# Performance work log

Hardware: AMD Instinct MI355X
Metric: run time of the kernel (lower is better)

Reference implementation:

```python
import jax, jax.numpy as jnp
import numpy as np

NUM_EXPERTS = 7
TRUNK_DIM = 64
HIDDEN = 64   # max(48, trunk_dim)
NUM_DEPTH_CLASSES = 3
BATCH = 262144


def setup_inputs() -> dict:
    key = jax.random.key(0)
    ks = jax.random.split(key, 8)
    trunk_feat = jax.random.normal(ks[0], (BATCH, TRUNK_DIM), dtype=jnp.float32)
    size_idx = jax.random.randint(ks[1], (BATCH,), 0, NUM_EXPERTS, dtype=jnp.int64)
    # Stacked expert MLP params: Linear(64,64) -> ReLU -> Linear(64,64) -> ReLU -> Linear(64,3)
    s1 = 1.0 / np.sqrt(TRUNK_DIM)
    s2 = 1.0 / np.sqrt(HIDDEN)
    W1 = jax.random.uniform(ks[2], (NUM_EXPERTS, TRUNK_DIM, HIDDEN), jnp.float32, -s1, s1)
    b1 = jax.random.uniform(ks[3], (NUM_EXPERTS, HIDDEN), jnp.float32, -s1, s1)
    W2 = jax.random.uniform(ks[4], (NUM_EXPERTS, HIDDEN, HIDDEN), jnp.float32, -s2, s2)
    b2 = jax.random.uniform(ks[5], (NUM_EXPERTS, HIDDEN), jnp.float32, -s2, s2)
    W3 = jax.random.uniform(ks[6], (NUM_EXPERTS, HIDDEN, NUM_DEPTH_CLASSES), jnp.float32, -s2, s2)
    b3 = jax.random.uniform(ks[7], (NUM_EXPERTS, NUM_DEPTH_CLASSES), jnp.float32, -s2, s2)
    return {"trunk_feat": trunk_feat, "size_idx": size_idx,
            "W1": W1, "b1": b1, "W2": W2, "b2": b2, "W3": W3, "b3": b3}


def _expert_mlp(x, W1, b1, W2, b2, W3, b3):
    # 3-layer MLP of one expert (dropout = identity in eval mode)
    h = jax.nn.relu(x @ W1 + b1)
    h = jax.nn.relu(h @ W2 + b2)
    return h @ W3 + b3  # [B, num_depth_classes]


def reference(trunk_feat, size_idx, W1, b1, W2, b2, W3, b3):
    # Hard routing (route_logits): rows with size_idx == e go through expert e;
    # expressed as masked accumulate so it is jit-friendly (no data-dependent shapes).
    B = trunk_feat.shape[0]
    logits = jnp.zeros((B, NUM_DEPTH_CLASSES), dtype=trunk_feat.dtype)
    for e in range(NUM_EXPERTS):  # fixed, small expert count
        le = _expert_mlp(trunk_feat, W1[e], b1[e], W2[e], b2[e], W3[e], b3[e])
        mask = (size_idx == e)[:, None]
        logits = logits + jnp.where(mask, le, jnp.zeros_like(le))
    probs = jax.nn.softmax(logits, axis=1)
    return logits, probs
```

## Files before the change

### kernel.cpp

```cpp
#include <hip/hip_runtime.h>
#include <stdint.h>

#define NE    7
#define DD    64
#define NDC   3
#define BLOCK 256
#define ROWS  128
#define NFRAG 18

typedef __fp16   half8 __attribute__((ext_vector_type(8)));
typedef float    f32x4 __attribute__((ext_vector_type(4)));
typedef uint32_t u32x4 __attribute__((ext_vector_type(4)));
typedef uint32_t u32x2 __attribute__((ext_vector_type(2)));
typedef __fp16   h2_t  __attribute__((ext_vector_type(2)));

__device__ __forceinline__ uint32_t pkrtz(float a, float b) {
  h2_t h = __builtin_amdgcn_cvt_pkrtz(a, b);
  return __builtin_bit_cast(uint32_t, h);
}

__device__ __forceinline__ f32x4 mfma16(u32x4 a, u32x4 b, f32x4 c) {
  return __builtin_amdgcn_mfma_f32_16x16x32_f16(
      __builtin_bit_cast(half8, a), __builtin_bit_cast(half8, b), c, 0, 0, 0);
}

__device__ __forceinline__ u32x4 relu_pack(f32x4 lo, f32x4 hi) {
  u32x4 t = { pkrtz(fmaxf(lo[0],0.f), fmaxf(lo[1],0.f)),
              pkrtz(fmaxf(lo[2],0.f), fmaxf(lo[3],0.f)),
              pkrtz(fmaxf(hi[0],0.f), fmaxf(hi[1],0.f)),
              pkrtz(fmaxf(hi[2],0.f), fmaxf(hi[3],0.f)) };
  return t;
}

__global__ __launch_bounds__(BLOCK) void pack_w2(
    const float* __restrict__ W1, const float* __restrict__ W2,
    const float* __restrict__ W3, uint32_t* __restrict__ ws) {
  __shared__ float wt[DD*DD];
  const int blk = blockIdx.x;
  const int e = blk >> 1, half = blk & 1;
  const float* Wsrc = (half ? W2 : W1) + (size_t)e*DD*DD;

  const float4* s4 = (const float4*)Wsrc;
  float4* d4 = (float4*)wt;
  #pragma unroll
  for (int i = 0; i < DD*DD/4/BLOCK; ++i)
    d4[i*BLOCK + threadIdx.x] = s4[i*BLOCK + threadIdx.x];
  __syncthreads();

  for (int idx = threadIdx.x; idx < 8*64; idx += BLOCK) {
    const int fl = idx >> 6, l = idx & 63;
    const int nt = fl >> 1, ks = fl & 1;
    const int n  = nt*16 + (l & 15), g = l >> 4;
    uint32_t dst[4];
    #pragma unroll
    for (int d = 0; d < 4; ++d) {
      float v[2];
      #pragma unroll
      for (int h = 0; h < 2; ++h) {
        const int kk = 16*(d>>1) + 4*g + 2*(d&1) + h;
        v[h] = wt[(32*ks + kk)*DD + n];
      }
      dst[d] = pkrtz(v[0], v[1]);
    }
    uint32_t* p = ws + ((size_t)(e*NFRAG + half*8 + fl)*64 + l)*4;
    p[0]=dst[0]; p[1]=dst[1]; p[2]=dst[2]; p[3]=dst[3];
  }

  if (half == 0) {
    const float* Wl2 = W3 + (size_t)e*DD*NDC;
    for (int idx = threadIdx.x; idx < 2*64; idx += BLOCK) {
      const int ks = idx >> 6, l = idx & 63;
      const int n  = l & 15, g = l >> 4;
      uint32_t dst[4];
      #pragma unroll
      for (int d = 0; d < 4; ++d) {
        float v[2];
        #pragma unroll
        for (int h = 0; h < 2; ++h) {
          const int kk = 16*(d>>1) + 4*g + 2*(d&1) + h;
          const int k  = 32*ks + kk;
          v[h] = (n < NDC) ? Wl2[k*NDC + n] : 0.0f;
        }
        dst[d] = pkrtz(v[0], v[1]);
      }
      uint32_t* p = ws + ((size_t)(e*NFRAG + 16 + ks)*64 + l)*4;
      p[0]=dst[0]; p[1]=dst[1]; p[2]=dst[2]; p[3]=dst[3];
    }
  }
}

__global__ __launch_bounds__(BLOCK, 4) void fused(
    const float* __restrict__ X, const int* __restrict__ S,
    const u32x4* __restrict__ wf,
    const float* __restrict__ b1, const float* __restrict__ b2,
    const float* __restrict__ b3,
    float* __restrict__ out, int B)
{
  __shared__ uint32_t pk[ROWS*32];
  __shared__ float    outbuf[ROWS*6];
  __shared__ uint16_t srt[ROWS];
  __shared__ int wcnt[2][NE];
  __shared__ int woff[2][NE];
  __shared__ int cnt[NE];

  const int tid  = threadIdx.x;
  const int wv   = tid >> 6, lane = tid & 63;
  const int r15  = lane & 15, g = lane >> 4;
  const int base = blockIdx.x * ROWS;

  int e_i = 0, myprefix = 0;
  if (wv < 2) {
    e_i = S[base + tid];
    unsigned long long mk[NE];
    #pragma unroll
    for (int e = 0; e < NE; ++e) mk[e] = __ballot(e_i == e);
    #pragma unroll
    for (int e = 0; e < NE; ++e)
      if (e_i == e) myprefix = __popcll(mk[e] & ((1ull << lane) - 1ull));
    if (lane < NE) wcnt[wv][lane] = __popcll(mk[lane]);
  }
  __syncthreads();

  if (tid == 0) {
    int acc = 0;
    for (int e = 0; e < NE; ++e) {
      const int s0 = acc;
      for (int w = 0; w < 2; ++w) { woff[w][e] = acc; acc += wcnt[w][e]; }
      cnt[e] = acc - s0;
    }
  }
  {
    const float4* Xb = (const float4*)(X + (size_t)base * DD);
    const int q     = lane & 15;
    const int rsub  = lane >> 4;
    const int ksq   = q >> 3, gq = q & 3, hq = (q >> 2) & 1;
    const int slotq = 4*ksq + gq;
    #pragma unroll
    for (int it = 0; it < 8; ++it) {
      const int r = wv*32 + it*4 + rsub;
      const float4 v = Xb[r*16 + q];
      u32x2 w2 = { pkrtz(v.x, v.y), pkrtz(v.z, v.w) };
      *(u32x2*)&pk[r*32 + ((slotq ^ (r & 7)) << 2) + hq*2] = w2;
    }
  }
  __syncthreads();

  if (tid < ROWS) srt[woff[wv][e_i] + myprefix] = (uint16_t)tid;
  __syncthreads();

  int pst[NE + 1];
  {
    int tp = 0;
    #pragma unroll
    for (int e = 0; e < NE; ++e) { pst[e] = tp; tp += (cnt[e] + 31) >> 5; }
    pst[NE] = tp;
  }

  for (int p = wv; p < pst[NE]; p += 4) {
    int e = 0;
    #pragma unroll
    for (int q2 = 1; q2 < NE; ++q2) if (p >= pst[q2]) e = q2;
    const int ch    = p - pst[e];
    const int m     = min(32, cnt[e] - ch*32);
    const int sbase = woff[0][e] + ch*32;
    const int njt   = (m > 16) ? 2 : 1;

    const u32x4* wse = wf + (size_t)e*NFRAG*64;

    u32x4 afA[8];
    #pragma unroll
    for (int f = 0; f < 8; ++f) afA[f] = wse[f*64 + lane];

    int lr[2] = {0, 0};
    u32x4 xf[2][2];
    #pragma unroll
    for (int jt = 0; jt < 2; ++jt) {
      if (jt >= njt) break;
      const int idx16 = min(jt*16 + r15, m - 1);
      lr[jt] = srt[sbase + idx16];
      xf[jt][0] = *(const u32x4*)&pk[lr[jt]*32 + (((    g) ^ (lr[jt] & 7)) << 2)];
      xf[jt][1] = *(const u32x4*)&pk[lr[jt]*32 + (((4 + g) ^ (lr[jt] & 7)) << 2)];
    }

    u32x4 h[2][2];
    #pragma unroll
    for (int jt = 0; jt < 2; ++jt) {
      if (jt >= njt) break;
      f32x4 c[4];
      #pragma unroll
      for (int nt = 0; nt < 4; ++nt) {
        const float4 bv = *(const float4*)(b1 + e*DD + nt*16 + 4*g);
        f32x4 acc = { bv.x, bv.y, bv.z, bv.w };
        acc = mfma16(afA[nt*2 + 0], xf[jt][0], acc);
        acc = mfma16(afA[nt*2 + 1], xf[jt][1], acc);
        c[nt] = acc;
      }
      h[jt][0] = relu_pack(c[0], c[1]);
      h[jt][1] = relu_pack(c[2], c[3]);
    }

    #pragma unroll
    for (int f = 0; f < 8; ++f) afA[f] = wse[(8 + f)*64 + lane];

    u32x4 t[2][2];
    #pragma unroll
    for (int jt = 0; jt < 2; ++jt) {
      if (jt >= njt) break;
      f32x4 c[4];
      #pragma unroll
      for (int nt = 0; nt < 4; ++nt) {
        const float4 bv = *(const float4*)(b2 + e*DD + nt*16 + 4*g);
        f32x4 acc = { bv.x, bv.y, bv.z, bv.w };
        acc = mfma16(afA[nt*2 + 0], h[jt][0], acc);
        acc = mfma16(afA[nt*2 + 1], h[jt][1], acc);
        c[nt] = acc;
      }
      t[jt][0] = relu_pack(c[0], c[1]);
      t[jt][1] = relu_pack(c[2], c[3]);
    }

    const u32x4 a30 = wse[16*64 + lane];
    const u32x4 a31 = wse[17*64 + lane];
    #pragma unroll
    for (int jt = 0; jt < 2; ++jt) {
      if (jt >= njt) break;
      f32x4 acc = { b3[e*NDC + 0], b3[e*NDC + 1], b3[e*NDC + 2], 0.f };
      acc = mfma16(a30, t[jt][0], acc);
      acc = mfma16(a31, t[jt][1], acc);
      if (g == 0 && (jt*16 + r15) < m) {
        const float l0 = acc[0], l1 = acc[1], l2 = acc[2];
        const float mx  = fmaxf(l0, fmaxf(l1, l2));
        const float p0  = __expf(l0 - mx);
        const float p1  = __expf(l1 - mx);
        const float p2  = __expf(l2 - mx);
        const float inv = 1.0f / (p0 + p1 + p2);
        float* ob = outbuf + lr[jt]*6;
        ob[0] = l0;      ob[1] = l1;      ob[2] = l2;
        ob[3] = p0*inv;  ob[4] = p1*inv;  ob[5] = p2*inv;
      }
    }
  }
  __syncthreads();

  for (int i = tid; i < ROWS*3; i += BLOCK) {
    const int r = i/3, c2 = i - r*3;
    out[(size_t)base*3 + i]                = outbuf[r*6 + c2];
    out[(size_t)B*3 + (size_t)base*3 + i]  = outbuf[r*6 + 3 + c2];
  }
}

extern "C" void kernel_launch(void* const* d_in, const int* in_sizes, int n_in,
                              void* d_out, int out_size, void* d_ws, size_t ws_size,
                              hipStream_t stream)
{
  const float* X  = (const float*)d_in[0];
  const int*   S  = (const int*)d_in[1];
  const float* W1 = (const float*)d_in[2];
  const float* B1 = (const float*)d_in[3];
  const float* W2 = (const float*)d_in[4];
  const float* B2 = (const float*)d_in[5];
  const float* W3 = (const float*)d_in[6];
  const float* B3 = (const float*)d_in[7];
  float* out = (float*)d_out;
  uint32_t* ws = (uint32_t*)d_ws;

  const int B = in_sizes[0] / DD;

  pack_w2<<<NE*2, BLOCK, 0, stream>>>(W1, W2, W3, ws);
  fused<<<B / ROWS, BLOCK, 0, stream>>>(X, S, (const u32x4*)ws,
                                        B1, B2, B3, out, B);
}
```

Before: 36.97 us.

## Split fused MoE kernel into global expert binning pass and per-bin MLP kernel

Replaces the single fused kernel, which grouped rows by expert only within each 128-row block, with two kernels. The first converts X to fp16 and scatters rows into global per-expert sub-bins using atomic counters. The second runs full 32-row MFMA tiles per bin with all weight fragments held in registers, writing outputs through a row-id indirection. This removes partially filled per-block expert tiles and repeated weight reloads, at the cost of an extra global round trip for the fp16 activations, an extra launch, scattered output writes, and a fixed bin capacity that could overflow on skewed inputs.

```diff
diff --git a/kernel.cpp b/kernel.cpp
--- a/kernel.cpp
+++ b/kernel.cpp
@@ -7,6 +7,12 @@
 #define BLOCK 256
 #define ROWS  128
 #define NFRAG 18
+#define NSUB  8
+#define NBIN  (NE*NSUB)
+#define CAP   5120
+#define WOFF  64
+#define BOFF  40960
+#define IOFF  (BOFF + NBIN*CAP*32)
 
 typedef __fp16   half8 __attribute__((ext_vector_type(8)));
 typedef float    f32x4 __attribute__((ext_vector_type(4)));
@@ -18,12 +24,10 @@
   h2_t h = __builtin_amdgcn_cvt_pkrtz(a, b);
   return __builtin_bit_cast(uint32_t, h);
 }
-
 __device__ __forceinline__ f32x4 mfma16(u32x4 a, u32x4 b, f32x4 c) {
   return __builtin_amdgcn_mfma_f32_16x16x32_f16(
       __builtin_bit_cast(half8, a), __builtin_bit_cast(half8, b), c, 0, 0, 0);
 }
-
 __device__ __forceinline__ u32x4 relu_pack(f32x4 lo, f32x4 hi) {
   u32x4 t = { pkrtz(fmaxf(lo[0],0.f), fmaxf(lo[1],0.f)),
               pkrtz(fmaxf(lo[2],0.f), fmaxf(lo[3],0.f)),
@@ -37,6 +41,7 @@
     const float* __restrict__ W3, uint32_t* __restrict__ ws) {
   __shared__ float wt[DD*DD];
   const int blk = blockIdx.x;
+  if (blk == 0 && threadIdx.x < WOFF) ws[threadIdx.x] = 0;
   const int e = blk >> 1, half = blk & 1;
   const float* Wsrc = (half ? W2 : W1) + (size_t)e*DD*DD;
 
@@ -62,7 +67,7 @@
       }
       dst[d] = pkrtz(v[0], v[1]);
     }
-    uint32_t* p = ws + ((size_t)(e*NFRAG + half*8 + fl)*64 + l)*4;
+    uint32_t* p = ws + WOFF + ((size_t)(e*NFRAG + half*8 + fl)*64 + l)*4;
     p[0]=dst[0]; p[1]=dst[1]; p[2]=dst[2]; p[3]=dst[3];
   }
 
@@ -78,35 +83,28 @@
         #pragma unroll
         for (int h = 0; h < 2; ++h) {
           const int kk = 16*(d>>1) + 4*g + 2*(d&1) + h;
-          const int k  = 32*ks + kk;
-          v[h] = (n < NDC) ? Wl2[k*NDC + n] : 0.0f;
+          v[h] = (n < NDC) ? Wl2[(32*ks + kk)*NDC + n] : 0.0f;
         }
         dst[d] = pkrtz(v[0], v[1]);
       }
-      uint32_t* p = ws + ((size_t)(e*NFRAG + 16 + ks)*64 + l)*4;
+      uint32_t* p = ws + WOFF + ((size_t)(e*NFRAG + 16 + ks)*64 + l)*4;
       p[0]=dst[0]; p[1]=dst[1]; p[2]=dst[2]; p[3]=dst[3];
     }
   }
 }
 
-__global__ __launch_bounds__(BLOCK, 4) void fused(
+__global__ __launch_bounds__(BLOCK) void k1_bin(
     const float* __restrict__ X, const int* __restrict__ S,
-    const u32x4* __restrict__ wf,
-    const float* __restrict__ b1, const float* __restrict__ b2,
-    const float* __restrict__ b3,
-    float* __restrict__ out, int B)
+    uint32_t* __restrict__ ws)
 {
-  __shared__ uint32_t pk[ROWS*32];
-  __shared__ float    outbuf[ROWS*6];
+  __shared__ __align__(16) uint32_t pk[ROWS*32];
   __shared__ uint16_t srt[ROWS];
-  __shared__ int wcnt[2][NE];
-  __shared__ int woff[2][NE];
-  __shared__ int cnt[NE];
-
-  const int tid  = threadIdx.x;
-  const int wv   = tid >> 6, lane = tid & 63;
-  const int r15  = lane & 15, g = lane >> 4;
+  __shared__ uint8_t  srtE[ROWS];
+  __shared__ int wcnt[2][NE], woff[2][NE], cnt[NE], bbase[NE];
+
+  const int tid = threadIdx.x, wv = tid >> 6, lane = tid & 63;
   const int base = blockIdx.x * ROWS;
+  const int sub  = blockIdx.x & (NSUB - 1);
 
   int e_i = 0, myprefix = 0;
   if (wv < 2) {
@@ -118,6 +116,21 @@
     for (int e = 0; e < NE; ++e)
       if (e_i == e) myprefix = __popcll(mk[e] & ((1ull << lane) - 1ull));
     if (lane < NE) wcnt[wv][lane] = __popcll(mk[lane]);
+  }
+
+  {
+    const float4* Xb = (const float4*)(X + (size_t)base * DD);
+    const int q     = lane & 15;
+    const int rsub  = lane >> 4;
+    const int slotq = 4*(q >> 3) + (q & 3);
+    const int hq    = (q >> 2) & 1;
+    #pragma unroll
+    for (int it = 0; it < 8; ++it) {
+      const int r = wv*32 + it*4 + rsub;
+      const float4 v = Xb[r*16 + q];
+      u32x2 w2 = { pkrtz(v.x, v.y), pkrtz(v.z, v.w) };
+      *(u32x2*)&pk[r*32 + ((slotq ^ (r & 7)) << 2) + hq*2] = w2;
+    }
   }
   __syncthreads();
 
@@ -129,123 +142,133 @@
       cnt[e] = acc - s0;
     }
   }
+  __syncthreads();
+
+  if (tid < NE) bbase[tid] = atomicAdd((int*)ws + tid*NSUB + sub, cnt[tid]);
+  if (tid < ROWS) {
+    srt [woff[wv][e_i] + myprefix] = (uint16_t)tid;
+    srtE[woff[wv][e_i] + myprefix] = (uint8_t)e_i;
+  }
+  __syncthreads();
+
   {
-    const float4* Xb = (const float4*)(X + (size_t)base * DD);
-    const int q     = lane & 15;
-    const int rsub  = lane >> 4;
-    const int ksq   = q >> 3, gq = q & 3, hq = (q >> 2) & 1;
-    const int slotq = 4*ksq + gq;
-    #pragma unroll
-    for (int it = 0; it < 8; ++it) {
-      const int r = wv*32 + it*4 + rsub;
-      const float4 v = Xb[r*16 + q];
-      u32x2 w2 = { pkrtz(v.x, v.y), pkrtz(v.z, v.w) };
-      *(u32x2*)&pk[r*32 + ((slotq ^ (r & 7)) << 2) + hq*2] = w2;
-    }
-  }
-  __syncthreads();
-
-  if (tid < ROWS) srt[woff[wv][e_i] + myprefix] = (uint16_t)tid;
-  __syncthreads();
-
-  int pst[NE + 1];
-  {
-    int tp = 0;
-    #pragma unroll
-    for (int e = 0; e < NE; ++e) { pst[e] = tp; tp += (cnt[e] + 31) >> 5; }
-    pst[NE] = tp;
-  }
-
-  for (int p = wv; p < pst[NE]; p += 4) {
-    int e = 0;
-    #pragma unroll
-    for (int q2 = 1; q2 < NE; ++q2) if (p >= pst[q2]) e = q2;
-    const int ch    = p - pst[e];
-    const int m     = min(32, cnt[e] - ch*32);
-    const int sbase = woff[0][e] + ch*32;
-    const int njt   = (m > 16) ? 2 : 1;
-
-    const u32x4* wse = wf + (size_t)e*NFRAG*64;
-
-    u32x4 afA[8];
-    #pragma unroll
-    for (int f = 0; f < 8; ++f) afA[f] = wse[f*64 + lane];
-
-    int lr[2] = {0, 0};
-    u32x4 xf[2][2];
+    const int i  = tid >> 1, hh = tid & 1;
+    const int lr = srt[i];
+    const int ee = srtE[i];
+    const int slot = bbase[ee] + (i - woff[0][ee]);
+    uint32_t* dstb = ws + BOFF + ((size_t)(ee*NSUB + sub)*CAP + slot)*32;
+    #pragma unroll
+    for (int j = 0; j < 4; ++j) {
+      const int ls = hh*4 + j;
+      const u32x4 v = *(const u32x4*)&pk[lr*32 + ((ls ^ (lr & 7)) << 2)];
+      *(u32x4*)(dstb + ls*4) = v;
+    }
+  }
+  if (tid < ROWS) {
+    const int ee = srtE[tid];
+    const int slot = bbase[ee] + (tid - woff[0][ee]);
+    ws[IOFF + (size_t)(ee*NSUB + sub)*CAP + slot] = base + srt[tid];
+  }
+}
+
+__global__ __launch_bounds__(BLOCK) void k2_mlp(
+    const uint32_t* __restrict__ ws,
+    const float* __restrict__ b1, const float* __restrict__ b2,
+    const float* __restrict__ b3,
+    float* __restrict__ out, int B)
+{
+  const int bin = blockIdx.y;
+  const int e   = bin >> 3;
+  const int cn  = ((const int*)ws)[bin];
+  const int tid = threadIdx.x;
+  const int wv = tid >> 6, lane = tid & 63;
+  const int r15 = lane & 15, g = lane >> 4;
+  const int rel0 = blockIdx.x*128 + wv*32;
+  if (rel0 >= cn) return;
+
+  const uint32_t* bdat = ws + BOFF + (size_t)bin*CAP*32;
+  const int*      ids  = (const int*)ws + IOFF + (size_t)bin*CAP;
+
+  const int m   = min(32, cn - rel0);
+  const int njt = (m > 16) ? 2 : 1;
+
+  int rid[2];
+  u32x4 xf[2][2];
+  #pragma unroll
+  for (int jt = 0; jt < 2; ++jt) {
+    if (jt >= njt) break;
+    const int rr = min(rel0 + jt*16 + r15, cn - 1);
+    rid[jt] = ids[rr];
+    xf[jt][0] = *(const u32x4*)(bdat + (size_t)rr*32 + g*4);
+    xf[jt][1] = *(const u32x4*)(bdat + (size_t)rr*32 + (4 + g)*4);
+  }
+
+  const u32x4* wse = (const u32x4*)(ws + WOFF) + (size_t)e*NFRAG*64;
+  u32x4 af[NFRAG];
+  #pragma unroll
+  for (int f = 0; f < NFRAG; ++f) af[f] = wse[f*64 + lane];
+
+  f32x4 c[4][2];
+  #pragma unroll
+  for (int nt = 0; nt < 4; ++nt) {
+    const float4 bv = *(const float4*)(b1 + e*DD + nt*16 + 4*g);
     #pragma unroll
     for (int jt = 0; jt < 2; ++jt) {
       if (jt >= njt) break;
-      const int idx16 = min(jt*16 + r15, m - 1);
-      lr[jt] = srt[sbase + idx16];
-      xf[jt][0] = *(const u32x4*)&pk[lr[jt]*32 + (((    g) ^ (lr[jt] & 7)) << 2)];
-      xf[jt][1] = *(const u32x4*)&pk[lr[jt]*32 + (((4 + g) ^ (lr[jt] & 7)) << 2)];
-    }
-
-    u32x4 h[2][2];
+      f32x4 acc = { bv.x, bv.y, bv.z, bv.w };
+      acc = mfma16(af[nt*2+0], xf[jt][0], acc);
+      acc = mfma16(af[nt*2+1], xf[jt][1], acc);
+      c[nt][jt] = acc;
+    }
+  }
+  u32x4 hf[2][2];
+  #pragma unroll
+  for (int jt = 0; jt < 2; ++jt) {
+    if (jt >= njt) break;
+    hf[jt][0] = relu_pack(c[0][jt], c[1][jt]);
+    hf[jt][1] = relu_pack(c[2][jt], c[3][jt]);
+  }
+
+  #pragma unroll
+  for (int nt = 0; nt < 4; ++nt) {
+    const float4 bv = *(const float4*)(b2 + e*DD + nt*16 + 4*g);
     #pragma unroll
     for (int jt = 0; jt < 2; ++jt) {
       if (jt >= njt) break;
-      f32x4 c[4];
-      #pragma unroll
-      for (int nt = 0; nt < 4; ++nt) {
-        const float4 bv = *(const float4*)(b1 + e*DD + nt*16 + 4*g);
-        f32x4 acc = { bv.x, bv.y, bv.z, bv.w };
-        acc = mfma16(afA[nt*2 + 0], xf[jt][0], acc);
-        acc = mfma16(afA[nt*2 + 1], xf[jt][1], acc);
-        c[nt] = acc;
-      }
-      h[jt][0] = relu_pack(c[0], c[1]);
-      h[jt][1] = relu_pack(c[2], c[3]);
-    }
-
-    #pragma unroll
-    for (int f = 0; f < 8; ++f) afA[f] = wse[(8 + f)*64 + lane];
-
-    u32x4 t[2][2];
-    #pragma unroll
-    for (int jt = 0; jt < 2; ++jt) {
-      if (jt >= njt) break;
-      f32x4 c[4];
-      #pragma unroll
-      for (int nt = 0; nt < 4; ++nt) {
-        const float4 bv = *(const float4*)(b2 + e*DD + nt*16 + 4*g);
-        f32x4 acc = { bv.x, bv.y, bv.z, bv.w };
-        acc = mfma16(afA[nt*2 + 0], h[jt][0], acc);
-        acc = mfma16(afA[nt*2 + 1], h[jt][1], acc);
-        c[nt] = acc;
-      }
-      t[jt][0] = relu_pack(c[0], c[1]);
-      t[jt][1] = relu_pack(c[2], c[3]);
-    }
-
-    const u32x4 a30 = wse[16*64 + lane];
-    const u32x4 a31 = wse[17*64 + lane];
-    #pragma unroll
-    for (int jt = 0; jt < 2; ++jt) {
-      if (jt >= njt) break;
-      f32x4 acc = { b3[e*NDC + 0], b3[e*NDC + 1], b3[e*NDC + 2], 0.f };
-      acc = mfma16(a30, t[jt][0], acc);
-      acc = mfma16(a31, t[jt][1], acc);
-      if (g == 0 && (jt*16 + r15) < m) {
-        const float l0 = acc[0], l1 = acc[1], l2 = acc[2];
-        const float mx  = fmaxf(l0, fmaxf(l1, l2));
-        const float p0  = __expf(l0 - mx);
-        const float p1  = __expf(l1 - mx);
-        const float p2  = __expf(l2 - mx);
-        const float inv = 1.0f / (p0 + p1 + p2);
-        float* ob = outbuf + lr[jt]*6;
-        ob[0] = l0;      ob[1] = l1;      ob[2] = l2;
-        ob[3] = p0*inv;  ob[4] = p1*inv;  ob[5] = p2*inv;
-      }
-    }
-  }
-  __syncthreads();
-
-  for (int i = tid; i < ROWS*3; i += BLOCK) {
-    const int r = i/3, c2 = i - r*3;
-    out[(size_t)base*3 + i]                = outbuf[r*6 + c2];
-    out[(size_t)B*3 + (size_t)base*3 + i]  = outbuf[r*6 + 3 + c2];
+      f32x4 acc = { bv.x, bv.y, bv.z, bv.w };
+      acc = mfma16(af[8+nt*2+0], hf[jt][0], acc);
+      acc = mfma16(af[8+nt*2+1], hf[jt][1], acc);
+      c[nt][jt] = acc;
+    }
+  }
+  u32x4 tf[2][2];
+  #pragma unroll
+  for (int jt = 0; jt < 2; ++jt) {
+    if (jt >= njt) break;
+    tf[jt][0] = relu_pack(c[0][jt], c[1][jt]);
+    tf[jt][1] = relu_pack(c[2][jt], c[3][jt]);
+  }
+
+  const float bb0 = b3[e*NDC+0], bb1 = b3[e*NDC+1], bb2 = b3[e*NDC+2];
+  #pragma unroll
+  for (int jt = 0; jt < 2; ++jt) {
+    if (jt >= njt) break;
+    f32x4 acc = { bb0, bb1, bb2, 0.f };
+    acc = mfma16(af[16], tf[jt][0], acc);
+    acc = mfma16(af[17], tf[jt][1], acc);
+    if (g == 0 && (jt*16 + r15) < m) {
+      const int row = rid[jt];
+      const float l0 = acc[0], l1 = acc[1], l2 = acc[2];
+      const float mx  = fmaxf(l0, fmaxf(l1, l2));
+      const float p0  = __expf(l0 - mx);
+      const float p1  = __expf(l1 - mx);
+      const float p2  = __expf(l2 - mx);
+      const float inv = 1.0f / (p0 + p1 + p2);
+      float* o = out + (size_t)row*3;
+      o[0] = l0; o[1] = l1; o[2] = l2;
+      float* pr = out + (size_t)B*3 + (size_t)row*3;
+      pr[0] = p0*inv; pr[1] = p1*inv; pr[2] = p2*inv;
+    }
   }
 }
 
@@ -267,6 +290,6 @@
   const int B = in_sizes[0] / DD;
 
   pack_w2<<<NE*2, BLOCK, 0, stream>>>(W1, W2, W3, ws);
-  fused<<<B / ROWS, BLOCK, 0, stream>>>(X, S, (const u32x4*)ws,
-                                        B1, B2, B3, out, B);
-}
+  k1_bin <<<B / ROWS, BLOCK, 0, stream>>>(X, S, ws);
+  k2_mlp <<<dim3(CAP/128, NBIN), BLOCK, 0, stream>>>(ws, B1, B2, B3, out, B);
+}
```

After: 76.24 us. 2.06x slower.

## Process two row tiles per block, prefetching the second tile during compute

Applied to the files above, without the earlier changes.

Each block now handles two 128-row tiles with double-buffered shared memory. The global loads of X and the routing indices for the second tile are issued before the first tile's compute, so memory latency overlaps the MFMA work. Several __syncthreads are replaced by a custom s_waitcnt lgkmcnt(0) plus s_barrier macro that does not wait on outstanding global loads. Register and LDS use rise and the occupancy hint drops from 4 to 3, and the grid is halved.

```diff
diff --git a/kernel.cpp b/kernel.cpp
--- a/kernel.cpp
+++ b/kernel.cpp
@@ -18,12 +18,10 @@
   h2_t h = __builtin_amdgcn_cvt_pkrtz(a, b);
   return __builtin_bit_cast(uint32_t, h);
 }
-
 __device__ __forceinline__ f32x4 mfma16(u32x4 a, u32x4 b, f32x4 c) {
   return __builtin_amdgcn_mfma_f32_16x16x32_f16(
       __builtin_bit_cast(half8, a), __builtin_bit_cast(half8, b), c, 0, 0, 0);
 }
-
 __device__ __forceinline__ u32x4 relu_pack(f32x4 lo, f32x4 hi) {
   u32x4 t = { pkrtz(fmaxf(lo[0],0.f), fmaxf(lo[1],0.f)),
               pkrtz(fmaxf(lo[2],0.f), fmaxf(lo[3],0.f)),
@@ -31,6 +29,11 @@
               pkrtz(fmaxf(hi[2],0.f), fmaxf(hi[3],0.f)) };
   return t;
 }
+#define LGKM_BAR() do {                                         \
+  asm volatile("s_waitcnt lgkmcnt(0)" ::: "memory");            \
+  __builtin_amdgcn_s_barrier();                                 \
+  __builtin_amdgcn_sched_barrier(0);                            \
+} while (0)
 
 __global__ __launch_bounds__(BLOCK) void pack_w2(
     const float* __restrict__ W1, const float* __restrict__ W2,
@@ -39,7 +42,6 @@
   const int blk = blockIdx.x;
   const int e = blk >> 1, half = blk & 1;
   const float* Wsrc = (half ? W2 : W1) + (size_t)e*DD*DD;
-
   const float4* s4 = (const float4*)Wsrc;
   float4* d4 = (float4*)wt;
   #pragma unroll
@@ -65,7 +67,6 @@
     uint32_t* p = ws + ((size_t)(e*NFRAG + half*8 + fl)*64 + l)*4;
     p[0]=dst[0]; p[1]=dst[1]; p[2]=dst[2]; p[3]=dst[3];
   }
-
   if (half == 0) {
     const float* Wl2 = W3 + (size_t)e*DD*NDC;
     for (int idx = threadIdx.x; idx < 2*64; idx += BLOCK) {
@@ -78,8 +79,7 @@
         #pragma unroll
         for (int h = 0; h < 2; ++h) {
           const int kk = 16*(d>>1) + 4*g + 2*(d&1) + h;
-          const int k  = 32*ks + kk;
-          v[h] = (n < NDC) ? Wl2[k*NDC + n] : 0.0f;
+          v[h] = (n < NDC) ? Wl2[(32*ks + kk)*NDC + n] : 0.0f;
         }
         dst[d] = pkrtz(v[0], v[1]);
       }
@@ -89,164 +89,194 @@
   }
 }
 
-__global__ __launch_bounds__(BLOCK, 4) void fused(
+__global__ __launch_bounds__(BLOCK, 3) void fused(
     const float* __restrict__ X, const int* __restrict__ S,
     const u32x4* __restrict__ wf,
     const float* __restrict__ b1, const float* __restrict__ b2,
     const float* __restrict__ b3,
     float* __restrict__ out, int B)
 {
-  __shared__ uint32_t pk[ROWS*32];
+  __shared__ uint32_t pk[2][ROWS*32];
   __shared__ float    outbuf[ROWS*6];
-  __shared__ uint16_t srt[ROWS];
-  __shared__ int wcnt[2][NE];
-  __shared__ int woff[2][NE];
-  __shared__ int cnt[NE];
+  __shared__ uint16_t srt[2][ROWS];
+  __shared__ int wcnt[2][2][NE], woff[2][2][NE], cnt[2][NE];
 
   const int tid  = threadIdx.x;
   const int wv   = tid >> 6, lane = tid & 63;
   const int r15  = lane & 15, g = lane >> 4;
-  const int base = blockIdx.x * ROWS;
-
-  int e_i = 0, myprefix = 0;
-  if (wv < 2) {
-    e_i = S[base + tid];
-    unsigned long long mk[NE];
+  const int q    = lane & 15, rsub = lane >> 4;
+  const int slotq = 4*(q >> 3) + (q & 3);
+  const int hq    = (q >> 2) & 1;
+  const int base0 = blockIdx.x * (2*ROWS);
+  const int base1 = base0 + ROWS;
+
+  auto ballots = [&](int cbase, int buf, int& e_o, int& p_o) {
+    if (wv < 2) {
+      e_o = S[cbase + tid];
+      unsigned long long mk[NE];
+      #pragma unroll
+      for (int e = 0; e < NE; ++e) mk[e] = __ballot(e_o == e);
+      #pragma unroll
+      for (int e = 0; e < NE; ++e)
+        if (e_o == e) p_o = __popcll(mk[e] & ((1ull << lane) - 1ull));
+      if (lane < NE) wcnt[buf][wv][lane] = __popcll(mk[lane]);
+    }
+  };
+  auto bload = [&](int cbase, float4* raw) {
+    const float4* Xb = (const float4*)(X + (size_t)cbase * DD);
     #pragma unroll
-    for (int e = 0; e < NE; ++e) mk[e] = __ballot(e_i == e);
-    #pragma unroll
-    for (int e = 0; e < NE; ++e)
-      if (e_i == e) myprefix = __popcll(mk[e] & ((1ull << lane) - 1ull));
-    if (lane < NE) wcnt[wv][lane] = __popcll(mk[lane]);
-  }
-  __syncthreads();
-
-  if (tid == 0) {
-    int acc = 0;
-    for (int e = 0; e < NE; ++e) {
-      const int s0 = acc;
-      for (int w = 0; w < 2; ++w) { woff[w][e] = acc; acc += wcnt[w][e]; }
-      cnt[e] = acc - s0;
-    }
-  }
-  {
-    const float4* Xb = (const float4*)(X + (size_t)base * DD);
-    const int q     = lane & 15;
-    const int rsub  = lane >> 4;
-    const int ksq   = q >> 3, gq = q & 3, hq = (q >> 2) & 1;
-    const int slotq = 4*ksq + gq;
+    for (int it = 0; it < 8; ++it)
+      raw[it] = Xb[(wv*32 + it*4 + rsub)*16 + q];
+  };
+  auto bwrite = [&](int buf, const float4* raw) {
     #pragma unroll
     for (int it = 0; it < 8; ++it) {
       const int r = wv*32 + it*4 + rsub;
-      const float4 v = Xb[r*16 + q];
-      u32x2 w2 = { pkrtz(v.x, v.y), pkrtz(v.z, v.w) };
-      *(u32x2*)&pk[r*32 + ((slotq ^ (r & 7)) << 2) + hq*2] = w2;
-    }
-  }
-  __syncthreads();
-
-  if (tid < ROWS) srt[woff[wv][e_i] + myprefix] = (uint16_t)tid;
-  __syncthreads();
-
-  int pst[NE + 1];
-  {
+      u32x2 w2 = { pkrtz(raw[it].x, raw[it].y), pkrtz(raw[it].z, raw[it].w) };
+      *(u32x2*)&pk[buf][r*32 + ((slotq ^ (r & 7)) << 2) + hq*2] = w2;
+    }
+  };
+  auto scan = [&](int buf) {
+    if (tid == 0) {
+      int acc = 0;
+      for (int e = 0; e < NE; ++e) {
+        const int s0 = acc;
+        for (int w = 0; w < 2; ++w) { woff[buf][w][e] = acc; acc += wcnt[buf][w][e]; }
+        cnt[buf][e] = acc - s0;
+      }
+    }
+  };
+  auto scatter = [&](int buf, int e_i, int pref) {
+    if (wv < 2) srt[buf][woff[buf][wv][e_i] + pref] = (uint16_t)tid;
+  };
+
+  auto compute = [&](int buf) {
+    int pst[NE + 1];
     int tp = 0;
     #pragma unroll
-    for (int e = 0; e < NE; ++e) { pst[e] = tp; tp += (cnt[e] + 31) >> 5; }
+    for (int e = 0; e < NE; ++e) { pst[e] = tp; tp += (cnt[buf][e] + 31) >> 5; }
     pst[NE] = tp;
-  }
-
-  for (int p = wv; p < pst[NE]; p += 4) {
-    int e = 0;
-    #pragma unroll
-    for (int q2 = 1; q2 < NE; ++q2) if (p >= pst[q2]) e = q2;
-    const int ch    = p - pst[e];
-    const int m     = min(32, cnt[e] - ch*32);
-    const int sbase = woff[0][e] + ch*32;
-    const int njt   = (m > 16) ? 2 : 1;
-
-    const u32x4* wse = wf + (size_t)e*NFRAG*64;
-
-    u32x4 afA[8];
-    #pragma unroll
-    for (int f = 0; f < 8; ++f) afA[f] = wse[f*64 + lane];
-
-    int lr[2] = {0, 0};
-    u32x4 xf[2][2];
-    #pragma unroll
-    for (int jt = 0; jt < 2; ++jt) {
-      if (jt >= njt) break;
-      const int idx16 = min(jt*16 + r15, m - 1);
-      lr[jt] = srt[sbase + idx16];
-      xf[jt][0] = *(const u32x4*)&pk[lr[jt]*32 + (((    g) ^ (lr[jt] & 7)) << 2)];
-      xf[jt][1] = *(const u32x4*)&pk[lr[jt]*32 + (((4 + g) ^ (lr[jt] & 7)) << 2)];
-    }
-
-    u32x4 h[2][2];
-    #pragma unroll
-    for (int jt = 0; jt < 2; ++jt) {
-      if (jt >= njt) break;
-      f32x4 c[4];
-      #pragma unroll
-      for (int nt = 0; nt < 4; ++nt) {
-        const float4 bv = *(const float4*)(b1 + e*DD + nt*16 + 4*g);
-        f32x4 acc = { bv.x, bv.y, bv.z, bv.w };
-        acc = mfma16(afA[nt*2 + 0], xf[jt][0], acc);
-        acc = mfma16(afA[nt*2 + 1], xf[jt][1], acc);
-        c[nt] = acc;
-      }
-      h[jt][0] = relu_pack(c[0], c[1]);
-      h[jt][1] = relu_pack(c[2], c[3]);
-    }
-
-    #pragma unroll
-    for (int f = 0; f < 8; ++f) afA[f] = wse[(8 + f)*64 + lane];
-
-    u32x4 t[2][2];
-    #pragma unroll
-    for (int jt = 0; jt < 2; ++jt) {
-      if (jt >= njt) break;
-      f32x4 c[4];
-      #pragma unroll
-      for (int nt = 0; nt < 4; ++nt) {
-        const float4 bv = *(const float4*)(b2 + e*DD + nt*16 + 4*g);
-        f32x4 acc = { bv.x, bv.y, bv.z, bv.w };
-        acc = mfma16(afA[nt*2 + 0], h[jt][0], acc);
-        acc = mfma16(afA[nt*2 + 1], h[jt][1], acc);
-        c[nt] = acc;
-      }
-      t[jt][0] = relu_pack(c[0], c[1]);
-      t[jt][1] = relu_pack(c[2], c[3]);
-    }
-
-    const u32x4 a30 = wse[16*64 + lane];
-    const u32x4 a31 = wse[17*64 + lane];
-    #pragma unroll
-    for (int jt = 0; jt < 2; ++jt) {
-      if (jt >= njt) break;
-      f32x4 acc = { b3[e*NDC + 0], b3[e*NDC + 1], b3[e*NDC + 2], 0.f };
-      acc = mfma16(a30, t[jt][0], acc);
-      acc = mfma16(a31, t[jt][1], acc);
-      if (g == 0 && (jt*16 + r15) < m) {
-        const float l0 = acc[0], l1 = acc[1], l2 = acc[2];
-        const float mx  = fmaxf(l0, fmaxf(l1, l2));
-        const float p0  = __expf(l0 - mx);
-        const float p1  = __expf(l1 - mx);
-        const float p2  = __expf(l2 - mx);
-        const float inv = 1.0f / (p0 + p1 + p2);
-        float* ob = outbuf + lr[jt]*6;
-        ob[0] = l0;      ob[1] = l1;      ob[2] = l2;
-        ob[3] = p0*inv;  ob[4] = p1*inv;  ob[5] = p2*inv;
-      }
-    }
-  }
+
+    for (int p = wv; p < pst[NE]; p += 4) {
+      int e = 0;
+      #pragma unroll
+      for (int q2 = 1; q2 < NE; ++q2) if (p >= pst[q2]) e = q2;
+      const int ch    = p - pst[e];
+      const int m     = min(32, cnt[buf][e] - ch*32);
+      const int sbase = woff[buf][0][e] + ch*32;
+      const int njt   = (m > 16) ? 2 : 1;
+
+      const u32x4* wse = wf + (size_t)e*NFRAG*64;
+      u32x4 afA[8];
+      #pragma unroll
+      for (int f = 0; f < 8; ++f) afA[f] = wse[f*64 + lane];
+
+      int lr[2] = {0, 0};
+      u32x4 xf[2][2];
+      #pragma unroll
+      for (int jt = 0; jt < 2; ++jt) {
+        if (jt >= njt) break;
+        const int idx16 = min(jt*16 + r15, m - 1);
+        lr[jt] = srt[buf][sbase + idx16];
+        xf[jt][0] = *(const u32x4*)&pk[buf][lr[jt]*32 + (((    g) ^ (lr[jt] & 7)) << 2)];
+        xf[jt][1] = *(const u32x4*)&pk[buf][lr[jt]*32 + (((4 + g) ^ (lr[jt] & 7)) << 2)];
+      }
+
+      u32x4 h[2][2];
+      #pragma unroll
+      for (int jt = 0; jt < 2; ++jt) {
+        if (jt >= njt) break;
+        f32x4 c[4];
+        #pragma unroll
+        for (int nt = 0; nt < 4; ++nt) {
+          const float4 bv = *(const float4*)(b1 + e*DD + nt*16 + 4*g);
+          f32x4 acc = { bv.x, bv.y, bv.z, bv.w };
+          acc = mfma16(afA[nt*2 + 0], xf[jt][0], acc);
+          acc = mfma16(afA[nt*2 + 1], xf[jt][1], acc);
+          c[nt] = acc;
+        }
+        h[jt][0] = relu_pack(c[0], c[1]);
+        h[jt][1] = relu_pack(c[2], c[3]);
+      }
+
+      #pragma unroll
+      for (int f = 0; f < 8; ++f) afA[f] = wse[(8 + f)*64 + lane];
+
+      u32x4 t[2][2];
+      #pragma unroll
+      for (int jt = 0; jt < 2; ++jt) {
+        if (jt >= njt) break;
+        f32x4 c[4];
+        #pragma unroll
+        for (int nt = 0; nt < 4; ++nt) {
+          const float4 bv = *(const float4*)(b2 + e*DD + nt*16 + 4*g);
+          f32x4 acc = { bv.x, bv.y, bv.z, bv.w };
+          acc = mfma16(afA[nt*2 + 0], h[jt][0], acc);
+          acc = mfma16(afA[nt*2 + 1], h[jt][1], acc);
+          c[nt] = acc;
+        }
+        t[jt][0] = relu_pack(c[0], c[1]);
+        t[jt][1] = relu_pack(c[2], c[3]);
+      }
+
+      const u32x4 a30 = wse[16*64 + lane];
+      const u32x4 a31 = wse[17*64 + lane];
+      #pragma unroll
+      for (int jt = 0; jt < 2; ++jt) {
+        if (jt >= njt) break;
+        f32x4 acc = { b3[e*NDC + 0], b3[e*NDC + 1], b3[e*NDC + 2], 0.f };
+        acc = mfma16(a30, t[jt][0], acc);
+        acc = mfma16(a31, t[jt][1], acc);
+        if (g == 0 && (jt*16 + r15) < m) {
+          const float l0 = acc[0], l1 = acc[1], l2 = acc[2];
+          const float mx  = fmaxf(l0, fmaxf(l1, l2));
+          const float p0  = __expf(l0 - mx);
+          const float p1  = __expf(l1 - mx);
+          const float p2  = __expf(l2 - mx);
+          const float inv = 1.0f / (p0 + p1 + p2);
+          float* ob = outbuf + lr[jt]*6;
+          ob[0] = l0;     ob[1] = l1;     ob[2] = l2;
+          ob[3] = p0*inv; ob[4] = p1*inv; ob[5] = p2*inv;
+        }
+      }
+    }
+  };
+
+  auto dout = [&](int cbase) {
+    for (int i = tid; i < ROWS*3; i += BLOCK) {
+      const int r = i/3, c2 = i - r*3;
+      out[(size_t)cbase*3 + i]                 = outbuf[r*6 + c2];
+      out[(size_t)B*3 + (size_t)cbase*3 + i]   = outbuf[r*6 + 3 + c2];
+    }
+  };
+
+  int e0 = 0, p0 = 0, e1 = 0, p1 = 0;
+  float4 raw[8];
+
+  ballots(base0, 0, e0, p0);
+  bload(base0, raw);
+  bwrite(0, raw);
   __syncthreads();
-
-  for (int i = tid; i < ROWS*3; i += BLOCK) {
-    const int r = i/3, c2 = i - r*3;
-    out[(size_t)base*3 + i]                = outbuf[r*6 + c2];
-    out[(size_t)B*3 + (size_t)base*3 + i]  = outbuf[r*6 + 3 + c2];
-  }
+  scan(0);
+  LGKM_BAR();
+  scatter(0, e0, p0);
+
+  ballots(base1, 1, e1, p1);
+  bload(base1, raw);
+  LGKM_BAR();
+
+  compute(0);
+  LGKM_BAR();
+  dout(base0);
+
+  bwrite(1, raw);
+  scan(1);
+  __syncthreads();
+  scatter(1, e1, p1);
+  LGKM_BAR();
+  compute(1);
+  LGKM_BAR();
+  dout(base1);
 }
 
 extern "C" void kernel_launch(void* const* d_in, const int* in_sizes, int n_in,
@@ -267,6 +297,6 @@
   const int B = in_sizes[0] / DD;
 
   pack_w2<<<NE*2, BLOCK, 0, stream>>>(W1, W2, W3, ws);
-  fused<<<B / ROWS, BLOCK, 0, stream>>>(X, S, (const u32x4*)ws,
-                                        B1, B2, B3, out, B);
-}
+  fused<<<B / (2*ROWS), BLOCK, 0, stream>>>(X, S, (const u32x4*)ws,
+                                            B1, B2, B3, out, B);
+}
```

New measurement: 41.93 us. 1.13x slower.

## Assign one wave per expert with register-resident weights and larger blocks

Applied to the files above, without the earlier changes.

The fused kernel now uses 448-thread blocks (7 waves) over 256 rows. Each wave is bound to one expert and preloads all 18 weight fragments into registers once, then loops over its expert's rows in 16-row tiles. This replaces the dynamic chunk-to-wave scheduling, which reloaded weights for every chunk. The trade-offs are load imbalance between waves when expert counts differ, higher register pressure from the 18 fragments against launch_bounds(…,4), and fewer blocks overall.

```diff
diff --git a/kernel.cpp b/kernel.cpp
--- a/kernel.cpp
+++ b/kernel.cpp
@@ -4,8 +4,8 @@
 #define NE    7
 #define DD    64
 #define NDC   3
-#define BLOCK 256
-#define ROWS  128
+#define BLOCK 448
+#define ROWS  256
 #define NFRAG 18
 
 typedef __fp16   half8 __attribute__((ext_vector_type(8)));
@@ -18,12 +18,10 @@
   h2_t h = __builtin_amdgcn_cvt_pkrtz(a, b);
   return __builtin_bit_cast(uint32_t, h);
 }
-
 __device__ __forceinline__ f32x4 mfma16(u32x4 a, u32x4 b, f32x4 c) {
   return __builtin_amdgcn_mfma_f32_16x16x32_f16(
       __builtin_bit_cast(half8, a), __builtin_bit_cast(half8, b), c, 0, 0, 0);
 }
-
 __device__ __forceinline__ u32x4 relu_pack(f32x4 lo, f32x4 hi) {
   u32x4 t = { pkrtz(fmaxf(lo[0],0.f), fmaxf(lo[1],0.f)),
               pkrtz(fmaxf(lo[2],0.f), fmaxf(lo[3],0.f)),
@@ -32,22 +30,21 @@
   return t;
 }
 
-__global__ __launch_bounds__(BLOCK) void pack_w2(
+__global__ __launch_bounds__(256) void pack_w2(
     const float* __restrict__ W1, const float* __restrict__ W2,
     const float* __restrict__ W3, uint32_t* __restrict__ ws) {
   __shared__ float wt[DD*DD];
   const int blk = blockIdx.x;
   const int e = blk >> 1, half = blk & 1;
   const float* Wsrc = (half ? W2 : W1) + (size_t)e*DD*DD;
-
   const float4* s4 = (const float4*)Wsrc;
   float4* d4 = (float4*)wt;
   #pragma unroll
-  for (int i = 0; i < DD*DD/4/BLOCK; ++i)
-    d4[i*BLOCK + threadIdx.x] = s4[i*BLOCK + threadIdx.x];
-  __syncthreads();
-
-  for (int idx = threadIdx.x; idx < 8*64; idx += BLOCK) {
+  for (int i = 0; i < DD*DD/4/256; ++i)
+    d4[i*256 + threadIdx.x] = s4[i*256 + threadIdx.x];
+  __syncthreads();
+
+  for (int idx = threadIdx.x; idx < 8*64; idx += 256) {
     const int fl = idx >> 6, l = idx & 63;
     const int nt = fl >> 1, ks = fl & 1;
     const int n  = nt*16 + (l & 15), g = l >> 4;
@@ -65,10 +62,9 @@
     uint32_t* p = ws + ((size_t)(e*NFRAG + half*8 + fl)*64 + l)*4;
     p[0]=dst[0]; p[1]=dst[1]; p[2]=dst[2]; p[3]=dst[3];
   }
-
   if (half == 0) {
     const float* Wl2 = W3 + (size_t)e*DD*NDC;
-    for (int idx = threadIdx.x; idx < 2*64; idx += BLOCK) {
+    for (int idx = threadIdx.x; idx < 2*64; idx += 256) {
       const int ks = idx >> 6, l = idx & 63;
       const int n  = l & 15, g = l >> 4;
       uint32_t dst[4];
@@ -78,8 +74,7 @@
         #pragma unroll
         for (int h = 0; h < 2; ++h) {
           const int kk = 16*(d>>1) + 4*g + 2*(d&1) + h;
-          const int k  = 32*ks + kk;
-          v[h] = (n < NDC) ? Wl2[k*NDC + n] : 0.0f;
+          v[h] = (n < NDC) ? Wl2[(32*ks + kk)*NDC + n] : 0.0f;
         }
         dst[d] = pkrtz(v[0], v[1]);
       }
@@ -99,153 +94,122 @@
   __shared__ uint32_t pk[ROWS*32];
   __shared__ float    outbuf[ROWS*6];
   __shared__ uint16_t srt[ROWS];
-  __shared__ int wcnt[2][NE];
-  __shared__ int woff[2][NE];
-  __shared__ int cnt[NE];
+  __shared__ int wcnt[4][NE], woff[4][NE], cnt[NE];
 
   const int tid  = threadIdx.x;
   const int wv   = tid >> 6, lane = tid & 63;
   const int r15  = lane & 15, g = lane >> 4;
   const int base = blockIdx.x * ROWS;
+  const int e    = wv;
+
+  const u32x4* wse = wf + (size_t)e*NFRAG*64;
+  u32x4 af[NFRAG];
+  #pragma unroll
+  for (int f = 0; f < NFRAG; ++f) af[f] = wse[f*64 + lane];
 
   int e_i = 0, myprefix = 0;
-  if (wv < 2) {
+  if (wv < 4) {
     e_i = S[base + tid];
     unsigned long long mk[NE];
     #pragma unroll
-    for (int e = 0; e < NE; ++e) mk[e] = __ballot(e_i == e);
-    #pragma unroll
-    for (int e = 0; e < NE; ++e)
-      if (e_i == e) myprefix = __popcll(mk[e] & ((1ull << lane) - 1ull));
+    for (int q2 = 0; q2 < NE; ++q2) mk[q2] = __ballot(e_i == q2);
+    #pragma unroll
+    for (int q2 = 0; q2 < NE; ++q2)
+      if (e_i == q2) myprefix = __popcll(mk[q2] & ((1ull << lane) - 1ull));
     if (lane < NE) wcnt[wv][lane] = __popcll(mk[lane]);
+  }
+
+  {
+    const float4* Xb = (const float4*)(X + (size_t)base * DD);
+    #pragma unroll
+    for (int ii = 0; ii < 10; ++ii) {
+      const int i = ii*BLOCK + tid;
+      if (ii == 9 && i >= ROWS*16) break;
+      const int r = i >> 4, q = i & 15;
+      const float4 v = Xb[i];
+      const int slotq = 4*(q >> 3) + (q & 3);
+      const int hq    = (q >> 2) & 1;
+      u32x2 w2 = { pkrtz(v.x, v.y), pkrtz(v.z, v.w) };
+      *(u32x2*)&pk[r*32 + ((slotq ^ (r & 7)) << 2) + hq*2] = w2;
+    }
   }
   __syncthreads();
 
   if (tid == 0) {
     int acc = 0;
-    for (int e = 0; e < NE; ++e) {
+    for (int q2 = 0; q2 < NE; ++q2) {
       const int s0 = acc;
-      for (int w = 0; w < 2; ++w) { woff[w][e] = acc; acc += wcnt[w][e]; }
-      cnt[e] = acc - s0;
-    }
-  }
-  {
-    const float4* Xb = (const float4*)(X + (size_t)base * DD);
-    const int q     = lane & 15;
-    const int rsub  = lane >> 4;
-    const int ksq   = q >> 3, gq = q & 3, hq = (q >> 2) & 1;
-    const int slotq = 4*ksq + gq;
-    #pragma unroll
-    for (int it = 0; it < 8; ++it) {
-      const int r = wv*32 + it*4 + rsub;
-      const float4 v = Xb[r*16 + q];
-      u32x2 w2 = { pkrtz(v.x, v.y), pkrtz(v.z, v.w) };
-      *(u32x2*)&pk[r*32 + ((slotq ^ (r & 7)) << 2) + hq*2] = w2;
-    }
-  }
-  __syncthreads();
-
-  if (tid < ROWS) srt[woff[wv][e_i] + myprefix] = (uint16_t)tid;
-  __syncthreads();
-
-  int pst[NE + 1];
-  {
-    int tp = 0;
-    #pragma unroll
-    for (int e = 0; e < NE; ++e) { pst[e] = tp; tp += (cnt[e] + 31) >> 5; }
-    pst[NE] = tp;
-  }
-
-  for (int p = wv; p < pst[NE]; p += 4) {
-    int e = 0;
-    #pragma unroll
-    for (int q2 = 1; q2 < NE; ++q2) if (p >= pst[q2]) e = q2;
-    const int ch    = p - pst[e];
-    const int m     = min(32, cnt[e] - ch*32);
-    const int sbase = woff[0][e] + ch*32;
-    const int njt   = (m > 16) ? 2 : 1;
-
-    const u32x4* wse = wf + (size_t)e*NFRAG*64;
-
-    u32x4 afA[8];
-    #pragma unroll
-    for (int f = 0; f < 8; ++f) afA[f] = wse[f*64 + lane];
-
-    int lr[2] = {0, 0};
-    u32x4 xf[2][2];
-    #pragma unroll
-    for (int jt = 0; jt < 2; ++jt) {
-      if (jt >= njt) break;
-      const int idx16 = min(jt*16 + r15, m - 1);
-      lr[jt] = srt[sbase + idx16];
-      xf[jt][0] = *(const u32x4*)&pk[lr[jt]*32 + (((    g) ^ (lr[jt] & 7)) << 2)];
-      xf[jt][1] = *(const u32x4*)&pk[lr[jt]*32 + (((4 + g) ^ (lr[jt] & 7)) << 2)];
-    }
-
-    u32x4 h[2][2];
-    #pragma unroll
-    for (int jt = 0; jt < 2; ++jt) {
-      if (jt >= njt) break;
-      f32x4 c[4];
-      #pragma unroll
-      for (int nt = 0; nt < 4; ++nt) {
-        const float4 bv = *(const float4*)(b1 + e*DD + nt*16 + 4*g);
-        f32x4 acc = { bv.x, bv.y, bv.z, bv.w };
-        acc = mfma16(afA[nt*2 + 0], xf[jt][0], acc);
-        acc = mfma16(afA[nt*2 + 1], xf[jt][1], acc);
-        c[nt] = acc;
-      }
-      h[jt][0] = relu_pack(c[0], c[1]);
-      h[jt][1] = relu_pack(c[2], c[3]);
-    }
-
-    #pragma unroll
-    for (int f = 0; f < 8; ++f) afA[f] = wse[(8 + f)*64 + lane];
-
-    u32x4 t[2][2];
-    #pragma unroll
-    for (int jt = 0; jt < 2; ++jt) {
-      if (jt >= njt) break;
-      f32x4 c[4];
-      #pragma unroll
-      for (int nt = 0; nt < 4; ++nt) {
-        const float4 bv = *(const float4*)(b2 + e*DD + nt*16 + 4*g);
-        f32x4 acc = { bv.x, bv.y, bv.z, bv.w };
-        acc = mfma16(afA[nt*2 + 0], h[jt][0], acc);
-        acc = mfma16(afA[nt*2 + 1], h[jt][1], acc);
-        c[nt] = acc;
-      }
-      t[jt][0] = relu_pack(c[0], c[1]);
-      t[jt][1] = relu_pack(c[2], c[3]);
-    }
-
-    const u32x4 a30 = wse[16*64 + lane];
-    const u32x4 a31 = wse[17*64 + lane];
-    #pragma unroll
-    for (int jt = 0; jt < 2; ++jt) {
-      if (jt >= njt) break;
-      f32x4 acc = { b3[e*NDC + 0], b3[e*NDC + 1], b3[e*NDC + 2], 0.f };
-      acc = mfma16(a30, t[jt][0], acc);
-      acc = mfma16(a31, t[jt][1], acc);
-      if (g == 0 && (jt*16 + r15) < m) {
-        const float l0 = acc[0], l1 = acc[1], l2 = acc[2];
-        const float mx  = fmaxf(l0, fmaxf(l1, l2));
-        const float p0  = __expf(l0 - mx);
-        const float p1  = __expf(l1 - mx);
-        const float p2  = __expf(l2 - mx);
-        const float inv = 1.0f / (p0 + p1 + p2);
-        float* ob = outbuf + lr[jt]*6;
-        ob[0] = l0;      ob[1] = l1;      ob[2] = l2;
-        ob[3] = p0*inv;  ob[4] = p1*inv;  ob[5] = p2*inv;
-      }
+      for (int w = 0; w < 4; ++w) { woff[w][q2] = acc; acc += wcnt[w][q2]; }
+      cnt[q2] = acc - s0;
+    }
+  }
+  __syncthreads();
+
+  if (wv < 4) srt[woff[wv][e_i] + myprefix] = (uint16_t)tid;
+  __syncthreads();
+
+  const int cn    = cnt[e];
+  const int sbase = woff[0][e];
+  const float4 bv1[4] = { *(const float4*)(b1 + e*DD +  0 + 4*g),
+                          *(const float4*)(b1 + e*DD + 16 + 4*g),
+                          *(const float4*)(b1 + e*DD + 32 + 4*g),
+                          *(const float4*)(b1 + e*DD + 48 + 4*g) };
+  const float4 bv2[4] = { *(const float4*)(b2 + e*DD +  0 + 4*g),
+                          *(const float4*)(b2 + e*DD + 16 + 4*g),
+                          *(const float4*)(b2 + e*DD + 32 + 4*g),
+                          *(const float4*)(b2 + e*DD + 48 + 4*g) };
+  const float bb0 = b3[e*NDC+0], bb1 = b3[e*NDC+1], bb2 = b3[e*NDC+2];
+
+  for (int r0 = 0; r0 < cn; r0 += 16) {
+    const int m  = cn - r0;
+    const int lr = srt[sbase + r0 + min(r15, m - 1)];
+
+    const u32x4 xf0 = *(const u32x4*)&pk[lr*32 + (((    g) ^ (lr & 7)) << 2)];
+    const u32x4 xf1 = *(const u32x4*)&pk[lr*32 + (((4 + g) ^ (lr & 7)) << 2)];
+
+    f32x4 c[4];
+    #pragma unroll
+    for (int nt = 0; nt < 4; ++nt) {
+      f32x4 acc = { bv1[nt].x, bv1[nt].y, bv1[nt].z, bv1[nt].w };
+      acc = mfma16(af[nt*2 + 0], xf0, acc);
+      acc = mfma16(af[nt*2 + 1], xf1, acc);
+      c[nt] = acc;
+    }
+    const u32x4 h0 = relu_pack(c[0], c[1]);
+    const u32x4 h1 = relu_pack(c[2], c[3]);
+
+    #pragma unroll
+    for (int nt = 0; nt < 4; ++nt) {
+      f32x4 acc = { bv2[nt].x, bv2[nt].y, bv2[nt].z, bv2[nt].w };
+      acc = mfma16(af[8 + nt*2 + 0], h0, acc);
+      acc = mfma16(af[8 + nt*2 + 1], h1, acc);
+      c[nt] = acc;
+    }
+    const u32x4 t0 = relu_pack(c[0], c[1]);
+    const u32x4 t1 = relu_pack(c[2], c[3]);
+
+    f32x4 acc = { bb0, bb1, bb2, 0.f };
+    acc = mfma16(af[16], t0, acc);
+    acc = mfma16(af[17], t1, acc);
+
+    if (g == 0 && r15 < m) {
+      const float l0 = acc[0], l1 = acc[1], l2 = acc[2];
+      const float mx  = fmaxf(l0, fmaxf(l1, l2));
+      const float p0  = __expf(l0 - mx);
+      const float p1  = __expf(l1 - mx);
+      const float p2  = __expf(l2 - mx);
+      const float inv = 1.0f / (p0 + p1 + p2);
+      float* ob = outbuf + lr*6;
+      ob[0] = l0;     ob[1] = l1;     ob[2] = l2;
+      ob[3] = p0*inv; ob[4] = p1*inv; ob[5] = p2*inv;
     }
   }
   __syncthreads();
 
   for (int i = tid; i < ROWS*3; i += BLOCK) {
     const int r = i/3, c2 = i - r*3;
-    out[(size_t)base*3 + i]                = outbuf[r*6 + c2];
-    out[(size_t)B*3 + (size_t)base*3 + i]  = outbuf[r*6 + 3 + c2];
+    out[(size_t)base*3 + i]               = outbuf[r*6 + c2];
+    out[(size_t)B*3 + (size_t)base*3 + i] = outbuf[r*6 + 3 + c2];
   }
 }
 
@@ -266,7 +230,7 @@
 
   const int B = in_sizes[0] / DD;
 
-  pack_w2<<<NE*2, BLOCK, 0, stream>>>(W1, W2, W3, ws);
+  pack_w2<<<NE*2, 256, 0, stream>>>(W1, W2, W3, ws);
   fused<<<B / ROWS, BLOCK, 0, stream>>>(X, S, (const u32x4*)ws,
                                         B1, B2, B3, out, B);
 }
```

Result: slower. 41.33 us (+11.8%).
